# Kernel optimization log

Hardware: AMD Instinct MI355X
Metric: run time of the kernel (lower is better)

Reference implementation:

```python
import jax, jax.numpy as jnp
import numpy as np

B, BINS, EMBED, HID, IND = 1, 500, 1024, 512, 128
POOL, MC_CROP, HIC_CROP = 5, 50, 10


def setup_inputs() -> dict:
    key = jax.random.key(0)
    ks = jax.random.split(key, 10)
    def w(k, shape, fan_in):
        return (jax.random.normal(k, shape, jnp.float32) / np.sqrt(fan_in)).astype(jnp.float32)
    return dict(
        x=jax.random.normal(ks[0], (B, BINS, EMBED), jnp.float32),
        # project MLP
        p_w1=w(ks[1], (EMBED, HID), EMBED), p_b1=jnp.zeros((HID,), jnp.float32),
        p_w2=w(ks[2], (HID, HID), HID), p_b2=jnp.zeros((HID,), jnp.float32),
        # pairattn_cop stub: per-pair linears (micro at full res, hic after 5x5 avg-pool)
        micro_w=w(ks[3], (HID, IND), HID), micro_b=jnp.zeros((IND,), jnp.float32),
        hic_w=w(ks[4], (HID, IND), HID), hic_b=jnp.zeros((IND,), jnp.float32),
        # prediction heads
        head_mc_w=w(ks[5], (IND, 2), IND), head_mc_b=jnp.zeros((2,), jnp.float32),
        head_ih_w1=w(ks[6], (IND, IND // 2), IND), head_ih_b1=jnp.zeros((IND // 2,), jnp.float32),
        head_ih_w2=w(ks[7], (IND // 2, 2), IND // 2), head_ih_b2=jnp.zeros((2,), jnp.float32),
        head_hic_w=w(ks[8], (IND, 3), IND), head_hic_b=jnp.zeros((3,), jnp.float32),
    )


def reference(x, p_w1, p_b1, p_w2, p_b2, micro_w, micro_b, hic_w, hic_b,
              head_mc_w, head_mc_b, head_ih_w1, head_ih_b1, head_ih_w2, head_ih_b2,
              head_hic_w, head_hic_b):
    # project: Linear -> ReLU -> Linear
    h = jax.nn.relu(x @ p_w1 + p_b1) @ p_w2 + p_b2            # [B, bins, HID]
    # output_head: fused pairwise outer-sum mean + scaled elementwise dot
    xi = h[:, :, None, :]                                      # [B, bins, 1, HID]
    xj = h[:, None, :, :]                                      # [B, 1, bins, HID]
    pair = (xi + xj) * 0.5 + xi * xj * (1.0 / np.sqrt(HID))    # [B, bins, bins, HID]
    # pairattn_cop stub
    micro = pair @ micro_w + micro_b                           # [B, bins, bins, IND]
    nb = BINS // POOL
    hic_in = pair.reshape(B, nb, POOL, nb, POOL, HID).mean(axis=(2, 4))  # [B, nb, nb, HID]
    hic = hic_in @ hic_w + hic_b                               # [B, nb, nb, IND]
    # prediction heads with crops
    mc = micro[:, MC_CROP:-MC_CROP, MC_CROP:-MC_CROP, :]       # [B, 400, 400, IND]
    out_mc = mc @ head_mc_w + head_mc_b
    out_ih = jax.nn.relu(mc @ head_ih_w1 + head_ih_b1) @ head_ih_w2 + head_ih_b2
    hc = hic[:, HIC_CROP:-HIC_CROP, HIC_CROP:-HIC_CROP, :]     # [B, 80, 80, IND]
    out_hic = hc @ head_hic_w + head_hic_b
    return (out_mc, out_ih, micro, out_hic)
```

## Files before the change

kernel.cpp:

```cpp
#include <hip/hip_runtime.h>

#define BINS 500
#define HID  512
#define INDD 128
#define PAIR_S 0.044194173824159216f

#define OFF_MC    0
#define OFF_IH    320000
#define OFF_MICRO 640000
#define OFF_HIC   32640000

#define WS_U     0
#define WS_MWT   64000
#define WS_HBF   96768
#define WS_H     256000
#define WS_HBAR  512000
#define WS_HWT   563200
#define WS_W1CT  595968

typedef __bf16 bf16;
typedef bf16 bf16x4 __attribute__((ext_vector_type(4)));
typedef bf16 bf16x8 __attribute__((ext_vector_type(8)));
typedef float f32x4 __attribute__((ext_vector_type(4)));

__device__ __forceinline__ bf16x8 join8(bf16x4 lo, bf16x4 hi) {
  return __builtin_shufflevector(lo, hi, 0, 1, 2, 3, 4, 5, 6, 7);
}
__device__ __forceinline__ bf16x4 cvt4(float a, float b, float c, float d) {
  bf16x4 r; r[0] = (bf16)a; r[1] = (bf16)b; r[2] = (bf16)c; r[3] = (bf16)d; return r;
}

__global__ __launch_bounds__(256, 2)
void gemm_ks(const float* __restrict__ A, const float* __restrict__ B,
             const float* __restrict__ abias, float* __restrict__ C,
             int M, int N, int K_per, int a_relu, float scale) {
  __shared__ float a_lds[64][36];
  __shared__ float bt_lds[64][36];
  const int t = threadIdx.x;
  const int w = t >> 6, l = t & 63;
  const int lr = l & 15, g = l >> 4;
  const int r0 = blockIdx.x * 64, n0 = blockIdx.y * 64;
  const int kbase = blockIdx.z * K_per;
  f32x4 acc[4] = {};
  for (int kq = 0; kq < K_per; kq += 32) {
    const int k0 = kbase + kq;
    {
      int row = t >> 2, kc = (t & 3) * 8;
      int gr = r0 + row; gr = gr < M ? gr : M - 1;
      const float* src = A + (size_t)gr * K_per * gridDim.z + k0 + kc;
      float4 v0 = *(const float4*)src;
      float4 v1 = *(const float4*)(src + 4);
      if (abias) {
        const float* bp = abias + k0 + kc;
        v0.x += bp[0]; v0.y += bp[1]; v0.z += bp[2]; v0.w += bp[3];
        v1.x += bp[4]; v1.y += bp[5]; v1.z += bp[6]; v1.w += bp[7];
        if (a_relu) {
          v0.x = fmaxf(v0.x, 0.f); v0.y = fmaxf(v0.y, 0.f);
          v0.z = fmaxf(v0.z, 0.f); v0.w = fmaxf(v0.w, 0.f);
          v1.x = fmaxf(v1.x, 0.f); v1.y = fmaxf(v1.y, 0.f);
          v1.z = fmaxf(v1.z, 0.f); v1.w = fmaxf(v1.w, 0.f);
        }
      }
      *(float4*)&a_lds[row][kc]     = v0;
      *(float4*)&a_lds[row][kc + 4] = v1;
    }
    {
      int n = t & 63, ks = (t >> 6) * 8;
      const float* src = B + (size_t)(k0 + ks) * N + n0 + n;
      #pragma unroll
      for (int s = 0; s < 8; s++) bt_lds[n][ks + s] = src[(size_t)s * N];
    }
    __syncthreads();
    bf16x8 ahi, alo;
    {
      int row = w * 16 + lr;
      float4 u0 = *(const float4*)&a_lds[row][g * 8];
      float4 u1 = *(const float4*)&a_lds[row][g * 8 + 4];
      float v[8] = {u0.x, u0.y, u0.z, u0.w, u1.x, u1.y, u1.z, u1.w};
      #pragma unroll
      for (int e = 0; e < 8; e++) {
        bf16 h = (bf16)v[e];
        ahi[e] = h; alo[e] = (bf16)(v[e] - (float)h);
      }
    }
    #pragma unroll
    for (int fn = 0; fn < 4; fn++) {
      int col = fn * 16 + lr;
      float4 u0 = *(const float4*)&bt_lds[col][g * 8];
      float4 u1 = *(const float4*)&bt_lds[col][g * 8 + 4];
      float v[8] = {u0.x, u0.y, u0.z, u0.w, u1.x, u1.y, u1.z, u1.w};
      bf16x8 bhi, blo;
      #pragma unroll
      for (int e = 0; e < 8; e++) {
        bf16 h = (bf16)v[e];
        bhi[e] = h; blo[e] = (bf16)(v[e] - (float)h);
      }
      acc[fn] = __builtin_amdgcn_mfma_f32_16x16x32_bf16(ahi, bhi, acc[fn], 0, 0, 0);
      acc[fn] = __builtin_amdgcn_mfma_f32_16x16x32_bf16(ahi, blo, acc[fn], 0, 0, 0);
      acc[fn] = __builtin_amdgcn_mfma_f32_16x16x32_bf16(alo, bhi, acc[fn], 0, 0, 0);
    }
    __syncthreads();
  }
  #pragma unroll
  for (int fn = 0; fn < 4; fn++) {
    int col = n0 + fn * 16 + lr;
    #pragma unroll
    for (int r = 0; r < 4; r++) {
      int row = r0 + w * 16 + g * 4 + r;
      if (row < M) atomicAdd(&C[(size_t)row * N + col], acc[fn][r] * scale);
    }
  }
}

__global__ void post_h(const float* __restrict__ h, const float* __restrict__ b2,
                       const float* __restrict__ micro_w,
                       const float* __restrict__ hic_w, const float* __restrict__ w_ih1,
                       const float* __restrict__ w_mc, float* __restrict__ ws) {
  int g = blockIdx.x * 256 + threadIdx.x;
  if (g < 256000) {
    bf16* hbf = (bf16*)(ws + WS_HBF);
    int k = g & (HID - 1);
    hbf[g] = (bf16)(h[g] + b2[k]);
  } else if (g < 256000 + 65536) {
    int gg = g - 256000;
    int n = gg >> 9, k = gg & 511;
    bf16* mwt = (bf16*)(ws + WS_MWT);
    mwt[gg] = (bf16)(PAIR_S * micro_w[k * INDD + n]);
  } else if (g < 256000 + 65536 + 51200) {
    int gg = g - (256000 + 65536);
    int a = gg >> 9, k = gg & (HID - 1);
    const float* p = h + (size_t)(a * 5) * HID + k;
    ws[WS_HBAR + gg] = 0.2f * (p[0] + p[HID] + p[2 * HID] + p[3 * HID] + p[4 * HID]) + b2[k];
  } else if (g < 256000 + 65536 + 51200 + 65536) {
    int gg = g - (256000 + 65536 + 51200);
    int n = gg >> 9, k = gg & 511;
    bf16* hwt = (bf16*)(ws + WS_HWT);
    hwt[gg] = (bf16)hic_w[k * INDD + n];
  } else if (g < 256000 + 65536 + 51200 + 65536 + 10240) {
    int gg = g - (256000 + 65536 + 51200 + 65536);
    int n = gg >> 7, k = gg & 127;
    float v = 0.f;
    if (n < 64) v = w_ih1[k * 64 + n];
    else if (n < 66) v = w_mc[k * 2 + (n - 64)];
    bf16* w1c = (bf16*)(ws + WS_W1CT);
    w1c[gg] = (bf16)v;
  }
}

__global__ __launch_bounds__(256, 3)
void fused_micro(const float* __restrict__ wsf, const float* __restrict__ micro_b,
                 float* __restrict__ out) {
  __shared__ bf16 Ht[2][128 * 32];
  __shared__ bf16 Bt[2][128 * 32];
  const int t = threadIdx.x;
  const int wv = t >> 6, l = t & 63;
  const int wj = wv >> 1, wn = wv & 1;
  const int lr = l & 15, g = l >> 4;
  const int i  = blockIdx.x;
  const int j0 = blockIdx.y * 128;
  const bf16* Hbf = (const bf16*)(wsf + WS_HBF);
  const bf16* mwt = (const bf16*)(wsf + WS_MWT);
  const float* U  = wsf + WS_U;
  const int bn = t >> 1, bh = t & 1;
  const int arow   = l >> 2;
  const int achunk = (l & 3) ^ ((l >> 3) & 3);
  const bf16* hbi = Hbf + (size_t)i * HID;
  f32x4 acc[4][4] = {};

  #pragma unroll
  for (int q = 0; q < 2; q++) {
    int row = wv * 32 + q * 16 + arow;
    int jj = j0 + row; jj = jj < BINS ? jj : BINS - 1;
    const bf16* src = Hbf + (size_t)jj * HID + achunk * 8;
    __builtin_amdgcn_global_load_lds(
        (const __attribute__((address_space(1))) void*)src,
        (__attribute__((address_space(3))) void*)(&Ht[0][(wv * 32 + q * 16) * 32]),
        16, 0, 0);
  }
  {
    bf16x8 w0 = *(const bf16x8*)(mwt + (size_t)bn * HID + bh * 16);
    bf16x8 w1 = *(const bf16x8*)(mwt + (size_t)bn * HID + bh * 16 + 8);
    bf16x8 h0 = *(const bf16x8*)(hbi + bh * 16);
    bf16x8 h1 = *(const bf16x8*)(hbi + bh * 16 + 8);
    bf16x8 o0, o1;
    #pragma unroll
    for (int e = 0; e < 8; e++) o0[e] = (bf16)((float)h0[e] * (float)w0[e]);
    #pragma unroll
    for (int e = 0; e < 8; e++) o1[e] = (bf16)((float)h1[e] * (float)w1[e]);
    const int sw = (bn >> 1) & 3;
    *(bf16x8*)(&Bt[0][0] + bn * 32 + ((bh * 2)     ^ sw) * 8) = o0;
    *(bf16x8*)(&Bt[0][0] + bn * 32 + ((bh * 2 + 1) ^ sw) * 8) = o1;
  }
  asm volatile("s_waitcnt vmcnt(0) lgkmcnt(0)" ::: "memory");
  __builtin_amdgcn_s_barrier();

  int cur = 0;
  for (int kt = 0; kt < 16; kt++) {
    const bf16* htc = &Ht[cur][0];
    const bf16* btc = &Bt[cur][0];
    bf16x8 w0, w1, h0, h1;
    if (kt < 15) {
      const int kn = (kt + 1) * 32;
      w0 = *(const bf16x8*)(mwt + (size_t)bn * HID + kn + bh * 16);
      w1 = *(const bf16x8*)(mwt + (size_t)bn * HID + kn + bh * 16 + 8);
      h0 = *(const bf16x8*)(hbi + kn + bh * 16);
      h1 = *(const bf16x8*)(hbi + kn + bh * 16 + 8);
      #pragma unroll
      for (int q = 0; q < 2; q++) {
        int row = wv * 32 + q * 16 + arow;
        int jj = j0 + row; jj = jj < BINS ? jj : BINS - 1;
        const bf16* src = Hbf + (size_t)jj * HID + kn + achunk * 8;
        __builtin_amdgcn_global_load_lds(
            (const __attribute__((address_space(1))) void*)src,
            (__attribute__((address_space(3))) void*)(&Ht[cur ^ 1][(wv * 32 + q * 16) * 32]),
            16, 0, 0);
      }
      asm volatile("s_waitcnt vmcnt(6)" ::: "memory");
    } else {
      asm volatile("s_waitcnt vmcnt(0)" ::: "memory");
    }
    bf16x8 af[4], bfr[4];
    const int s = g ^ ((lr >> 1) & 3);
    #pragma unroll
    for (int fm = 0; fm < 4; fm++)
      af[fm] = *(const bf16x8*)(htc + (wj * 64 + fm * 16 + lr) * 32 + s * 8);
    #pragma unroll
    for (int fn = 0; fn < 4; fn++)
      bfr[fn] = *(const bf16x8*)(btc + (wn * 64 + fn * 16 + lr) * 32 + s * 8);
    #pragma unroll
    for (int fm = 0; fm < 4; fm++)
      #pragma unroll
      for (int fn = 0; fn < 4; fn++)
        acc[fm][fn] = __builtin_amdgcn_mfma_f32_16x16x32_bf16(af[fm], bfr[fn], acc[fm][fn], 0, 0, 0);
    if (kt < 15) {
      bf16x8 o0, o1;
      #pragma unroll
      for (int e = 0; e < 8; e++) o0[e] = (bf16)((float)h0[e] * (float)w0[e]);
      #pragma unroll
      for (int e = 0; e < 8; e++) o1[e] = (bf16)((float)h1[e] * (float)w1[e]);
      bf16* btn = &Bt[cur ^ 1][0];
      const int sw = (bn >> 1) & 3;
      *(bf16x8*)(btn + bn * 32 + ((bh * 2)     ^ sw) * 8) = o0;
      *(bf16x8*)(btn + bn * 32 + ((bh * 2 + 1) ^ sw) * 8) = o1;
    }
    asm volatile("s_waitcnt lgkmcnt(0)" ::: "memory");
    __builtin_amdgcn_s_barrier();
    cur ^= 1;
  }

  float Ui[4];
  #pragma unroll
  for (int fn = 0; fn < 4; fn++) {
    int n = wn * 64 + fn * 16 + lr;
    Ui[fn] = U[(size_t)i * INDD + n] + micro_b[n];
  }
  #pragma unroll
  for (int fm = 0; fm < 4; fm++) {
    #pragma unroll
    for (int r = 0; r < 4; r++) {
      int j = j0 + wj * 64 + fm * 16 + g * 4 + r;
      if (j < BINS) {
        const float* Uj = U + (size_t)j * INDD;
        size_t base = (size_t)OFF_MICRO + ((size_t)i * BINS + j) * INDD;
        #pragma unroll
        for (int fn = 0; fn < 4; fn++) {
          int n = wn * 64 + fn * 16 + lr;
          out[base + n] = acc[fm][fn][r] + Ui[fn] + Uj[n];
        }
      }
    }
  }
}

__global__ __launch_bounds__(256, 2)
void heads_kernel(const float* __restrict__ micro, const float* __restrict__ wsf,
                  const float* __restrict__ b1, const float* __restrict__ w2,
                  const float* __restrict__ bmc, const float* __restrict__ b2,
                  float* __restrict__ out) {
  __shared__ bf16 a_lds[256][36];
  __shared__ bf16 bt_lds[80][132];
  const int t = threadIdx.x;
  const int wv = t >> 6, l = t & 63;
  const int lr = l & 15, g = l >> 4;
  const int mm0 = blockIdx.x * 256;
  const bf16* w1c = (const bf16*)(wsf + WS_W1CT);
  for (int c = t; c < 1280; c += 256) {
    int n = c >> 4, part = c & 15;
    bf16x8 v = *(const bf16x8*)(w1c + n * 128 + part * 8);
    *(bf16x4*)&bt_lds[n][part * 8]     = __builtin_shufflevector(v, v, 0, 1, 2, 3);
    *(bf16x4*)&bt_lds[n][part * 8 + 4] = __builtin_shufflevector(v, v, 4, 5, 6, 7);
  }
  f32x4 acc[4][5] = {};
  const int mm = mm0 + t;
  const int ii = 50 + mm / 400, jj = 50 + mm % 400;
  const float* arow = micro + (size_t)(ii * BINS + jj) * INDD;
  for (int kt = 0; kt < 4; kt++) {
    {
      const float* src = arow + kt * 32;
      #pragma unroll
      for (int c = 0; c < 4; c++) {
        float4 v0 = *(const float4*)(src + c * 8);
        float4 v1 = *(const float4*)(src + c * 8 + 4);
        *(bf16x4*)&a_lds[t][c * 8]     = cvt4(v0.x, v0.y, v0.z, v0.w);
        *(bf16x4*)&a_lds[t][c * 8 + 4] = cvt4(v1.x, v1.y, v1.z, v1.w);
      }
    }
    __syncthreads();
    bf16x8 af[4], bfr[5];
    #pragma unroll
    for (int fm = 0; fm < 4; fm++) {
      int row = wv * 64 + fm * 16 + lr;
      af[fm] = join8(*(const bf16x4*)&a_lds[row][g * 8],
                     *(const bf16x4*)&a_lds[row][g * 8 + 4]);
    }
    #pragma unroll
    for (int fn = 0; fn < 5; fn++) {
      int n = fn * 16 + lr;
      bfr[fn] = join8(*(const bf16x4*)&bt_lds[n][kt * 32 + g * 8],
                      *(const bf16x4*)&bt_lds[n][kt * 32 + g * 8 + 4]);
    }
    #pragma unroll
    for (int fm = 0; fm < 4; fm++)
      #pragma unroll
      for (int fn = 0; fn < 5; fn++)
        acc[fm][fn] = __builtin_amdgcn_mfma_f32_16x16x32_bf16(af[fm], bfr[fn], acc[fm][fn], 0, 0, 0);
    __syncthreads();
  }
  float w2a[4], w2b[4], b1v[4];
  #pragma unroll
  for (int fn = 0; fn < 4; fn++) {
    int q = fn * 16 + lr;
    w2a[fn] = w2[q * 2]; w2b[fn] = w2[q * 2 + 1]; b1v[fn] = b1[q];
  }
  float bm = (lr < 2) ? bmc[lr] : 0.f;
  float b2a = b2[0], b2bv = b2[1];
  #pragma unroll
  for (int fm = 0; fm < 4; fm++) {
    #pragma unroll
    for (int r = 0; r < 4; r++) {
      int m = wv * 64 + fm * 16 + g * 4 + r;
      float s0 = 0.f, s1 = 0.f;
      #pragma unroll
      for (int fn = 0; fn < 4; fn++) {
        float v = fmaxf(acc[fm][fn][r] + b1v[fn], 0.f);
        s0 += v * w2a[fn]; s1 += v * w2b[fn];
      }
      #pragma unroll
      for (int mk = 1; mk < 16; mk <<= 1) {
        s0 += __shfl_xor(s0, mk);
        s1 += __shfl_xor(s1, mk);
      }
      size_t mo = (size_t)(mm0 + m);
      if (lr == 0) {
        out[OFF_IH + mo * 2]     = s0 + b2a;
        out[OFF_IH + mo * 2 + 1] = s1 + b2bv;
      }
      if (lr < 2) out[OFF_MC + mo * 2 + lr] = acc[fm][4][r] + bm;
    }
  }
}

__device__ __forceinline__ bf16x4 pair4(float4 a, float4 b) {
  bf16x4 r;
  r[0] = (bf16)((a.x + b.x) * 0.5f + a.x * b.x * PAIR_S);
  r[1] = (bf16)((a.y + b.y) * 0.5f + a.y * b.y * PAIR_S);
  r[2] = (bf16)((a.z + b.z) * 0.5f + a.z * b.z * PAIR_S);
  r[3] = (bf16)((a.w + b.w) * 0.5f + a.w * b.w * PAIR_S);
  return r;
}

__global__ __launch_bounds__(256, 2)
void hic_kernel(const float* __restrict__ hbar, const float* __restrict__ wsf,
                const float* __restrict__ hicb, const float* __restrict__ whic,
                const float* __restrict__ bhic, float* __restrict__ out) {
  __shared__ float ha_lds[16][36];
  __shared__ float hb_lds[16][36];
  __shared__ bf16 pair_lds[256][36];
  __shared__ bf16 bt_lds[128][36];
  const int t = threadIdx.x;
  const int wv = t >> 6, l = t & 63;
  const int lr = l & 15, g = l >> 4;
  const int a0 = 10 + blockIdx.x * 16, b0 = 10 + blockIdx.y * 16;
  const bf16* hwt = (const bf16*)(wsf + WS_HWT);
  f32x4 acc[4][8] = {};
  for (int kt = 0; kt < 16; kt++) {
    const int k0 = kt * 32;
    if (t < 64) {
      int row = t >> 2, c = (t & 3) * 8;
      const float* src = hbar + (size_t)(a0 + row) * HID + k0 + c;
      *(float4*)&ha_lds[row][c]     = *(const float4*)src;
      *(float4*)&ha_lds[row][c + 4] = *(const float4*)(src + 4);
    } else if (t < 128) {
      int tt = t - 64;
      int row = tt >> 2, c = (tt & 3) * 8;
      const float* src = hbar + (size_t)(b0 + row) * HID + k0 + c;
      *(float4*)&hb_lds[row][c]     = *(const float4*)src;
      *(float4*)&hb_lds[row][c + 4] = *(const float4*)(src + 4);
    } else {
      int tt = t - 128;
      #pragma unroll
      for (int rep = 0; rep < 4; rep++) {
        int chunk = tt * 4 + rep;
        int n = chunk >> 2, part = chunk & 3;
        bf16x8 v = *(const bf16x8*)(hwt + (size_t)n * HID + k0 + part * 8);
        *(bf16x4*)&bt_lds[n][part * 8]     = __builtin_shufflevector(v, v, 0, 1, 2, 3);
        *(bf16x4*)&bt_lds[n][part * 8 + 4] = __builtin_shufflevector(v, v, 4, 5, 6, 7);
      }
    }
    __syncthreads();
    {
      int m = t;
      const float* pa = &ha_lds[m >> 4][0];
      const float* pb = &hb_lds[m & 15][0];
      #pragma unroll
      for (int c = 0; c < 4; c++) {
        float4 av0 = *(const float4*)(pa + c * 8);
        float4 av1 = *(const float4*)(pa + c * 8 + 4);
        float4 bv0 = *(const float4*)(pb + c * 8);
        float4 bv1 = *(const float4*)(pb + c * 8 + 4);
        *(bf16x4*)&pair_lds[m][c * 8]     = pair4(av0, bv0);
        *(bf16x4*)&pair_lds[m][c * 8 + 4] = pair4(av1, bv1);
      }
    }
    __syncthreads();
    bf16x8 af[4], bfr[8];
    #pragma unroll
    for (int fm = 0; fm < 4; fm++) {
      int row = wv * 64 + fm * 16 + lr;
      af[fm] = join8(*(const bf16x4*)&pair_lds[row][g * 8],
                     *(const bf16x4*)&pair_lds[row][g * 8 + 4]);
    }
    #pragma unroll
    for (int fn = 0; fn < 8; fn++) {
      int col = fn * 16 + lr;
      bfr[fn] = join8(*(const bf16x4*)&bt_lds[col][g * 8],
                      *(const bf16x4*)&bt_lds[col][g * 8 + 4]);
    }
    #pragma unroll
    for (int fm = 0; fm < 4; fm++)
      #pragma unroll
      for (int fn = 0; fn < 8; fn++)
        acc[fm][fn] = __builtin_amdgcn_mfma_f32_16x16x32_bf16(af[fm], bfr[fn], acc[fm][fn], 0, 0, 0);
    __syncthreads();
  }
  float wh0[8], wh1[8], wh2[8], hbv[8];
  #pragma unroll
  for (int fn = 0; fn < 8; fn++) {
    int n = fn * 16 + lr;
    wh0[fn] = whic[n * 3]; wh1[fn] = whic[n * 3 + 1]; wh2[fn] = whic[n * 3 + 2];
    hbv[fn] = hicb[n];
  }
  float bh0 = bhic[0], bh1 = bhic[1], bh2 = bhic[2];
  #pragma unroll
  for (int fm = 0; fm < 4; fm++) {
    #pragma unroll
    for (int r = 0; r < 4; r++) {
      int m = wv * 64 + fm * 16 + g * 4 + r;
      float s0 = 0.f, s1 = 0.f, s2 = 0.f;
      #pragma unroll
      for (int fn = 0; fn < 8; fn++) {
        float v = acc[fm][fn][r] + hbv[fn];
        s0 += v * wh0[fn]; s1 += v * wh1[fn]; s2 += v * wh2[fn];
      }
      #pragma unroll
      for (int mk = 1; mk < 16; mk <<= 1) {
        s0 += __shfl_xor(s0, mk);
        s1 += __shfl_xor(s1, mk);
        s2 += __shfl_xor(s2, mk);
      }
      if (lr == 0) {
        int aa = a0 + (m >> 4) - 10, bb = b0 + (m & 15) - 10;
        size_t o = (size_t)OFF_HIC + (size_t)(aa * 80 + bb) * 3;
        out[o] = s0 + bh0; out[o + 1] = s1 + bh1; out[o + 2] = s2 + bh2;
      }
    }
  }
}

extern "C" void kernel_launch(void* const* d_in, const int* in_sizes, int n_in,
                              void* d_out, int out_size, void* d_ws, size_t ws_size,
                              hipStream_t stream) {
  (void)in_sizes; (void)n_in; (void)out_size; (void)ws_size;
  const float* x    = (const float*)d_in[0];
  const float* pw1  = (const float*)d_in[1];
  const float* pb1  = (const float*)d_in[2];
  const float* pw2  = (const float*)d_in[3];
  const float* pb2  = (const float*)d_in[4];
  const float* mw   = (const float*)d_in[5];
  const float* mb   = (const float*)d_in[6];
  const float* hw   = (const float*)d_in[7];
  const float* hb   = (const float*)d_in[8];
  const float* wmc  = (const float*)d_in[9];
  const float* bmc  = (const float*)d_in[10];
  const float* wih1 = (const float*)d_in[11];
  const float* bih1 = (const float*)d_in[12];
  const float* wih2 = (const float*)d_in[13];
  const float* bih2 = (const float*)d_in[14];
  const float* whic = (const float*)d_in[15];
  const float* bhic = (const float*)d_in[16];
  float* out = (float*)d_out;
  float* ws  = (float*)d_ws;

  hipMemsetAsync(ws, 0, 256000 * sizeof(float), stream);
  hipMemsetAsync(ws + WS_H, 0, 256000 * sizeof(float), stream);
  gemm_ks<<<dim3(8, 8, 4), 256, 0, stream>>>(x, pw1, nullptr, ws, 500, 512, 256, 0, 1.f);
  gemm_ks<<<dim3(8, 8, 2), 256, 0, stream>>>(ws, pw2, pb1, ws + WS_H, 500, 512, 256, 1, 1.f);
  hipMemsetAsync(ws + WS_U, 0, 64000 * sizeof(float), stream);
  post_h<<<1752, 256, 0, stream>>>(ws + WS_H, pb2, mw, hw, wih1, wmc, ws);
  gemm_ks<<<dim3(8, 2, 4), 256, 0, stream>>>(ws + WS_H, mw, pb2, ws + WS_U, 500, 128, 128, 0, 0.5f);
  fused_micro<<<dim3(500, 4), 256, 0, stream>>>(ws, mb, out);
  heads_kernel<<<625, 256, 0, stream>>>(out + OFF_MICRO, ws, bih1, wih2, bmc, bih2, out);
  hic_kernel<<<dim3(5, 5), 256, 0, stream>>>(ws + WS_HBAR, ws, hb, whic, bhic, out);
}
```

Measured before the change: 171.0 us.

## Precompute per-row scaled micro weights and stream them via global_load_lds

```diff
diff --git a/kernel.cpp b/kernel.cpp
--- a/kernel.cpp
+++ b/kernel.cpp
@@ -17,6 +17,8 @@
 #define WS_HBAR  512000
 #define WS_HWT   563200
 #define WS_W1CT  595968
+#define WS_BP    601088
+#define WS_TOTAL_FLOATS (601088 + 8388608)
 
 typedef __bf16 bf16;
 typedef bf16 bf16x4 __attribute__((ext_vector_type(4)));
@@ -28,6 +30,13 @@
 }
 __device__ __forceinline__ bf16x4 cvt4(float a, float b, float c, float d) {
   bf16x4 r; r[0] = (bf16)a; r[1] = (bf16)b; r[2] = (bf16)c; r[3] = (bf16)d; return r;
+}
+
+__global__ void zero_init(float* __restrict__ ws) {
+  int idx = (blockIdx.x * 256 + threadIdx.x) * 4;
+  float4 z = {0.f, 0.f, 0.f, 0.f};
+  *(float4*)(ws + idx) = z;
+  *(float4*)(ws + WS_H + idx) = z;
 }
 
 __global__ __launch_bounds__(256, 2)
@@ -144,12 +153,131 @@
     else if (n < 66) v = w_mc[k * 2 + (n - 64)];
     bf16* w1c = (bf16*)(ws + WS_W1CT);
     w1c[gg] = (bf16)v;
+  } else if (g < 256000 + 65536 + 51200 + 65536 + 10240 + 64000) {
+    int gg = g - (256000 + 65536 + 51200 + 65536 + 10240);
+    ws[WS_U + gg] = 0.f;
+  }
+}
+
+__global__ void bp_gen(const float* __restrict__ wsf, float* __restrict__ wso) {
+  const bf16* hbf = (const bf16*)(wsf + WS_HBF);
+  const bf16* mwt = (const bf16*)(wsf + WS_MWT);
+  bf16* bp = (bf16*)(wso + WS_BP);
+  int gid = blockIdx.x * 256 + threadIdx.x;
+  int i  = gid >> 13;
+  int rem = gid & 8191;
+  int n  = rem >> 6;
+  int kc = (rem & 63) * 8;
+  bf16x8 hv = *(const bf16x8*)(hbf + (size_t)i * HID + kc);
+  bf16x8 wv = *(const bf16x8*)(mwt + (size_t)n * HID + kc);
+  bf16x8 o;
+  #pragma unroll
+  for (int e = 0; e < 8; e++) o[e] = (bf16)((float)hv[e] * (float)wv[e]);
+  *(bf16x8*)(bp + (size_t)i * 65536 + (size_t)n * HID + kc) = o;
+}
+
+__global__ __launch_bounds__(256, 4)
+void fused_micro_pre(const float* __restrict__ wsf, const float* __restrict__ micro_b,
+                     float* __restrict__ out) {
+  __shared__ bf16 Ht[2][128 * 32];
+  __shared__ bf16 Bt[2][128 * 32];
+  const int t = threadIdx.x;
+  const int wv = t >> 6, l = t & 63;
+  const int wj = wv >> 1, wn = wv & 1;
+  const int lr = l & 15, g = l >> 4;
+  const int i  = blockIdx.x;
+  const int j0 = blockIdx.y * 128;
+  const bf16* Hbf = (const bf16*)(wsf + WS_HBF);
+  const bf16* bpi = (const bf16*)(wsf + WS_BP) + (size_t)i * 65536;
+  const float* U  = wsf + WS_U;
+  const int arow   = l >> 2;
+  const int achunk = (l & 3) ^ ((l >> 3) & 3);
+  f32x4 acc[4][4] = {};
+
+  #pragma unroll
+  for (int q = 0; q < 2; q++) {
+    int row = wv * 32 + q * 16 + arow;
+    int jj = j0 + row; jj = jj < BINS ? jj : BINS - 1;
+    __builtin_amdgcn_global_load_lds(
+        (const __attribute__((address_space(1))) void*)(Hbf + (size_t)jj * HID + achunk * 8),
+        (__attribute__((address_space(3))) void*)(&Ht[0][(wv * 32 + q * 16) * 32]),
+        16, 0, 0);
+    __builtin_amdgcn_global_load_lds(
+        (const __attribute__((address_space(1))) void*)(bpi + (size_t)row * HID + achunk * 8),
+        (__attribute__((address_space(3))) void*)(&Bt[0][(wv * 32 + q * 16) * 32]),
+        16, 0, 0);
+  }
+  asm volatile("s_waitcnt vmcnt(0)" ::: "memory");
+  __builtin_amdgcn_s_barrier();
+
+  int cur = 0;
+  for (int kt = 0; kt < 16; kt++) {
+    const bf16* htc = &Ht[cur][0];
+    const bf16* btc = &Bt[cur][0];
+    if (kt < 15) {
+      const int kn = (kt + 1) * 32;
+      #pragma unroll
+      for (int q = 0; q < 2; q++) {
+        int row = wv * 32 + q * 16 + arow;
+        int jj = j0 + row; jj = jj < BINS ? jj : BINS - 1;
+        __builtin_amdgcn_global_load_lds(
+            (const __attribute__((address_space(1))) void*)(Hbf + (size_t)jj * HID + kn + achunk * 8),
+            (__attribute__((address_space(3))) void*)(&Ht[cur ^ 1][(wv * 32 + q * 16) * 32]),
+            16, 0, 0);
+        __builtin_amdgcn_global_load_lds(
+            (const __attribute__((address_space(1))) void*)(bpi + (size_t)row * HID + kn + achunk * 8),
+            (__attribute__((address_space(3))) void*)(&Bt[cur ^ 1][(wv * 32 + q * 16) * 32]),
+            16, 0, 0);
+      }
+      asm volatile("s_waitcnt vmcnt(4)" ::: "memory");
+    } else {
+      asm volatile("s_waitcnt vmcnt(0)" ::: "memory");
+    }
+    bf16x8 af[4], bfr[4];
+    const int s = g ^ ((lr >> 1) & 3);
+    #pragma unroll
+    for (int fm = 0; fm < 4; fm++)
+      af[fm] = *(const bf16x8*)(htc + (wj * 64 + fm * 16 + lr) * 32 + s * 8);
+    #pragma unroll
+    for (int fn = 0; fn < 4; fn++)
+      bfr[fn] = *(const bf16x8*)(btc + (wn * 64 + fn * 16 + lr) * 32 + s * 8);
+    #pragma unroll
+    for (int fm = 0; fm < 4; fm++)
+      #pragma unroll
+      for (int fn = 0; fn < 4; fn++)
+        acc[fm][fn] = __builtin_amdgcn_mfma_f32_16x16x32_bf16(af[fm], bfr[fn], acc[fm][fn], 0, 0, 0);
+    asm volatile("s_waitcnt lgkmcnt(0)" ::: "memory");
+    __builtin_amdgcn_s_barrier();
+    cur ^= 1;
+  }
+
+  float Ui[4];
+  #pragma unroll
+  for (int fn = 0; fn < 4; fn++) {
+    int n = wn * 64 + fn * 16 + lr;
+    Ui[fn] = U[(size_t)i * INDD + n] + micro_b[n];
+  }
+  #pragma unroll
+  for (int fm = 0; fm < 4; fm++) {
+    #pragma unroll
+    for (int r = 0; r < 4; r++) {
+      int j = j0 + wj * 64 + fm * 16 + g * 4 + r;
+      if (j < BINS) {
+        const float* Uj = U + (size_t)j * INDD;
+        size_t base = (size_t)OFF_MICRO + ((size_t)i * BINS + j) * INDD;
+        #pragma unroll
+        for (int fn = 0; fn < 4; fn++) {
+          int n = wn * 64 + fn * 16 + lr;
+          out[base + n] = acc[fm][fn][r] + Ui[fn] + Uj[n];
+        }
+      }
+    }
   }
 }
 
 __global__ __launch_bounds__(256, 3)
-void fused_micro(const float* __restrict__ wsf, const float* __restrict__ micro_b,
-                 float* __restrict__ out) {
+void fused_micro_fb(const float* __restrict__ wsf, const float* __restrict__ micro_b,
+                    float* __restrict__ out) {
   __shared__ bf16 Ht[2][128 * 32];
   __shared__ bf16 Bt[2][128 * 32];
   const int t = threadIdx.x;
@@ -171,9 +299,8 @@
   for (int q = 0; q < 2; q++) {
     int row = wv * 32 + q * 16 + arow;
     int jj = j0 + row; jj = jj < BINS ? jj : BINS - 1;
-    const bf16* src = Hbf + (size_t)jj * HID + achunk * 8;
     __builtin_amdgcn_global_load_lds(
-        (const __attribute__((address_space(1))) void*)src,
+        (const __attribute__((address_space(1))) void*)(Hbf + (size_t)jj * HID + achunk * 8),
         (__attribute__((address_space(3))) void*)(&Ht[0][(wv * 32 + q * 16) * 32]),
         16, 0, 0);
   }
@@ -209,9 +336,8 @@
       for (int q = 0; q < 2; q++) {
         int row = wv * 32 + q * 16 + arow;
         int jj = j0 + row; jj = jj < BINS ? jj : BINS - 1;
-        const bf16* src = Hbf + (size_t)jj * HID + kn + achunk * 8;
         __builtin_amdgcn_global_load_lds(
-            (const __attribute__((address_space(1))) void*)src,
+            (const __attribute__((address_space(1))) void*)(Hbf + (size_t)jj * HID + kn + achunk * 8),
             (__attribute__((address_space(3))) void*)(&Ht[cur ^ 1][(wv * 32 + q * 16) * 32]),
             16, 0, 0);
       }
@@ -480,7 +606,7 @@
 extern "C" void kernel_launch(void* const* d_in, const int* in_sizes, int n_in,
                               void* d_out, int out_size, void* d_ws, size_t ws_size,
                               hipStream_t stream) {
-  (void)in_sizes; (void)n_in; (void)out_size; (void)ws_size;
+  (void)in_sizes; (void)n_in; (void)out_size;
   const float* x    = (const float*)d_in[0];
   const float* pw1  = (const float*)d_in[1];
   const float* pb1  = (const float*)d_in[2];
@@ -500,15 +626,16 @@
   const float* bhic = (const float*)d_in[16];
   float* out = (float*)d_out;
   float* ws  = (float*)d_ws;
-
-  hipMemsetAsync(ws, 0, 256000 * sizeof(float), stream);
-  hipMemsetAsync(ws + WS_H, 0, 256000 * sizeof(float), stream);
+  const bool use_bp = ws_size >= (size_t)WS_TOTAL_FLOATS * sizeof(float);
+
+  zero_init<<<250, 256, 0, stream>>>(ws);
   gemm_ks<<<dim3(8, 8, 4), 256, 0, stream>>>(x, pw1, nullptr, ws, 500, 512, 256, 0, 1.f);
   gemm_ks<<<dim3(8, 8, 2), 256, 0, stream>>>(ws, pw2, pb1, ws + WS_H, 500, 512, 256, 1, 1.f);
-  hipMemsetAsync(ws + WS_U, 0, 64000 * sizeof(float), stream);
-  post_h<<<1752, 256, 0, stream>>>(ws + WS_H, pb2, mw, hw, wih1, wmc, ws);
+  post_h<<<2252, 256, 0, stream>>>(ws + WS_H, pb2, mw, hw, wih1, wmc, ws);
+  if (use_bp) bp_gen<<<16384, 256, 0, stream>>>(ws, ws);
   gemm_ks<<<dim3(8, 2, 4), 256, 0, stream>>>(ws + WS_H, mw, pb2, ws + WS_U, 500, 128, 128, 0, 0.5f);
-  fused_micro<<<dim3(500, 4), 256, 0, stream>>>(ws, mb, out);
+  if (use_bp) fused_micro_pre<<<dim3(500, 4), 256, 0, stream>>>(ws, mb, out);
+  else        fused_micro_fb<<<dim3(500, 4), 256, 0, stream>>>(ws, mb, out);
   heads_kernel<<<625, 256, 0, stream>>>(out + OFF_MICRO, ws, bih1, wih2, bmc, bih2, out);
   hic_kernel<<<dim3(5, 5), 256, 0, stream>>>(ws + WS_HBAR, ws, hb, whic, bhic, out);
 }
```

Result: slower. 183.1 us (+7.0%).

## Fuse prediction heads into micro GEMM epilogue and replace memsets with kernels

Applied to the files above, without the earlier changes.

```diff
diff --git a/kernel.cpp b/kernel.cpp
--- a/kernel.cpp
+++ b/kernel.cpp
@@ -28,6 +28,13 @@
 }
 __device__ __forceinline__ bf16x4 cvt4(float a, float b, float c, float d) {
   bf16x4 r; r[0] = (bf16)a; r[1] = (bf16)b; r[2] = (bf16)c; r[3] = (bf16)d; return r;
+}
+
+__global__ void zero_init(float* __restrict__ ws) {
+  int idx = (blockIdx.x * 256 + threadIdx.x) * 4;
+  float4 z = {0.f, 0.f, 0.f, 0.f};
+  *(float4*)(ws + idx) = z;
+  *(float4*)(ws + WS_H + idx) = z;
 }
 
 __global__ __launch_bounds__(256, 2)
@@ -144,14 +151,18 @@
     else if (n < 66) v = w_mc[k * 2 + (n - 64)];
     bf16* w1c = (bf16*)(ws + WS_W1CT);
     w1c[gg] = (bf16)v;
+  } else if (g < 256000 + 65536 + 51200 + 65536 + 10240 + 64000) {
+    int gg = g - (256000 + 65536 + 51200 + 65536 + 10240);
+    ws[WS_U + gg] = 0.f;
   }
 }
 
 __global__ __launch_bounds__(256, 3)
-void fused_micro(const float* __restrict__ wsf, const float* __restrict__ micro_b,
-                 float* __restrict__ out) {
-  __shared__ bf16 Ht[2][128 * 32];
-  __shared__ bf16 Bt[2][128 * 32];
+void fused_micro_heads(const float* __restrict__ wsf, const float* __restrict__ micro_b,
+                       const float* __restrict__ b1, const float* __restrict__ w2,
+                       const float* __restrict__ bmc, const float* __restrict__ b2,
+                       float* __restrict__ out) {
+  __shared__ bf16 smem[16384];
   const int t = threadIdx.x;
   const int wv = t >> 6, l = t & 63;
   const int wj = wv >> 1, wn = wv & 1;
@@ -171,10 +182,9 @@
   for (int q = 0; q < 2; q++) {
     int row = wv * 32 + q * 16 + arow;
     int jj = j0 + row; jj = jj < BINS ? jj : BINS - 1;
-    const bf16* src = Hbf + (size_t)jj * HID + achunk * 8;
     __builtin_amdgcn_global_load_lds(
-        (const __attribute__((address_space(1))) void*)src,
-        (__attribute__((address_space(3))) void*)(&Ht[0][(wv * 32 + q * 16) * 32]),
+        (const __attribute__((address_space(1))) void*)(Hbf + (size_t)jj * HID + achunk * 8),
+        (__attribute__((address_space(3))) void*)(smem + (wv * 32 + q * 16) * 32),
         16, 0, 0);
   }
   {
@@ -188,16 +198,16 @@
     #pragma unroll
     for (int e = 0; e < 8; e++) o1[e] = (bf16)((float)h1[e] * (float)w1[e]);
     const int sw = (bn >> 1) & 3;
-    *(bf16x8*)(&Bt[0][0] + bn * 32 + ((bh * 2)     ^ sw) * 8) = o0;
-    *(bf16x8*)(&Bt[0][0] + bn * 32 + ((bh * 2 + 1) ^ sw) * 8) = o1;
+    *(bf16x8*)(smem + 8192 + bn * 32 + ((bh * 2)     ^ sw) * 8) = o0;
+    *(bf16x8*)(smem + 8192 + bn * 32 + ((bh * 2 + 1) ^ sw) * 8) = o1;
   }
   asm volatile("s_waitcnt vmcnt(0) lgkmcnt(0)" ::: "memory");
   __builtin_amdgcn_s_barrier();
 
   int cur = 0;
   for (int kt = 0; kt < 16; kt++) {
-    const bf16* htc = &Ht[cur][0];
-    const bf16* btc = &Bt[cur][0];
+    const bf16* htc = smem + cur * 4096;
+    const bf16* btc = smem + 8192 + cur * 4096;
     bf16x8 w0, w1, h0, h1;
     if (kt < 15) {
       const int kn = (kt + 1) * 32;
@@ -209,10 +219,9 @@
       for (int q = 0; q < 2; q++) {
         int row = wv * 32 + q * 16 + arow;
         int jj = j0 + row; jj = jj < BINS ? jj : BINS - 1;
-        const bf16* src = Hbf + (size_t)jj * HID + kn + achunk * 8;
         __builtin_amdgcn_global_load_lds(
-            (const __attribute__((address_space(1))) void*)src,
-            (__attribute__((address_space(3))) void*)(&Ht[cur ^ 1][(wv * 32 + q * 16) * 32]),
+            (const __attribute__((address_space(1))) void*)(Hbf + (size_t)jj * HID + kn + achunk * 8),
+            (__attribute__((address_space(3))) void*)(smem + (cur ^ 1) * 4096 + (wv * 32 + q * 16) * 32),
             16, 0, 0);
       }
       asm volatile("s_waitcnt vmcnt(6)" ::: "memory");
@@ -238,7 +247,7 @@
       for (int e = 0; e < 8; e++) o0[e] = (bf16)((float)h0[e] * (float)w0[e]);
       #pragma unroll
       for (int e = 0; e < 8; e++) o1[e] = (bf16)((float)h1[e] * (float)w1[e]);
-      bf16* btn = &Bt[cur ^ 1][0];
+      bf16* btn = smem + 8192 + (cur ^ 1) * 4096;
       const int sw = (bn >> 1) & 3;
       *(bf16x8*)(btn + bn * 32 + ((bh * 2)     ^ sw) * 8) = o0;
       *(bf16x8*)(btn + bn * 32 + ((bh * 2 + 1) ^ sw) * 8) = o1;
@@ -258,104 +267,82 @@
   for (int fm = 0; fm < 4; fm++) {
     #pragma unroll
     for (int r = 0; r < 4; r++) {
-      int j = j0 + wj * 64 + fm * 16 + g * 4 + r;
-      if (j < BINS) {
-        const float* Uj = U + (size_t)j * INDD;
-        size_t base = (size_t)OFF_MICRO + ((size_t)i * BINS + j) * INDD;
+      int j_local = wj * 64 + fm * 16 + g * 4 + r;
+      int j = j0 + j_local;
+      int jc = j < BINS ? j : BINS - 1;
+      const float* Uj = U + (size_t)jc * INDD;
+      size_t base = (size_t)OFF_MICRO + ((size_t)i * BINS + jc) * INDD;
+      #pragma unroll
+      for (int fn = 0; fn < 4; fn++) {
+        int n = wn * 64 + fn * 16 + lr;
+        float vv = acc[fm][fn][r] + Ui[fn] + Uj[n];
+        if (j < BINS) out[base + n] = vv;
+        smem[j_local * 128 + ((((n >> 3) ^ (j_local & 7))) << 3) + (n & 7)] = (bf16)vv;
+      }
+    }
+  }
+  asm volatile("s_waitcnt lgkmcnt(0)" ::: "memory");
+  __builtin_amdgcn_s_barrier();
+
+  if (i >= 50 && i < 450) {
+    const bf16* w1c = (const bf16*)(wsf + WS_W1CT);
+    f32x4 acc2[2][5] = {};
+    const int jg = wv * 32;
+    #pragma unroll
+    for (int kt2 = 0; kt2 < 4; kt2++) {
+      const int k0 = kt2 * 32;
+      bf16x8 bfr[5];
+      #pragma unroll
+      for (int fn = 0; fn < 5; fn++) {
+        int q = fn * 16 + lr;
+        bfr[fn] = *(const bf16x8*)(w1c + q * 128 + k0 + g * 8);
+      }
+      bf16x8 af2[2];
+      #pragma unroll
+      for (int s16 = 0; s16 < 2; s16++) {
+        int row = jg + s16 * 16 + lr;
+        int chunk = (k0 >> 3) + g;
+        af2[s16] = *(const bf16x8*)(smem + row * 128 + ((chunk ^ (row & 7)) << 3));
+      }
+      #pragma unroll
+      for (int s16 = 0; s16 < 2; s16++)
+        #pragma unroll
+        for (int fn = 0; fn < 5; fn++)
+          acc2[s16][fn] = __builtin_amdgcn_mfma_f32_16x16x32_bf16(af2[s16], bfr[fn], acc2[s16][fn], 0, 0, 0);
+    }
+    float w2a[4], w2b[4], b1v[4];
+    #pragma unroll
+    for (int fn = 0; fn < 4; fn++) {
+      int q = fn * 16 + lr;
+      w2a[fn] = w2[q * 2]; w2b[fn] = w2[q * 2 + 1]; b1v[fn] = b1[q];
+    }
+    float bm = (lr < 2) ? bmc[lr] : 0.f;
+    float b2a = b2[0], b2bv = b2[1];
+    #pragma unroll
+    for (int s16 = 0; s16 < 2; s16++) {
+      #pragma unroll
+      for (int r = 0; r < 4; r++) {
+        int j = j0 + jg + s16 * 16 + g * 4 + r;
+        float s0 = 0.f, s1 = 0.f;
         #pragma unroll
         for (int fn = 0; fn < 4; fn++) {
-          int n = wn * 64 + fn * 16 + lr;
-          out[base + n] = acc[fm][fn][r] + Ui[fn] + Uj[n];
+          float v = fmaxf(acc2[s16][fn][r] + b1v[fn], 0.f);
+          s0 += v * w2a[fn]; s1 += v * w2b[fn];
         }
-      }
-    }
-  }
-}
-
-__global__ __launch_bounds__(256, 2)
-void heads_kernel(const float* __restrict__ micro, const float* __restrict__ wsf,
-                  const float* __restrict__ b1, const float* __restrict__ w2,
-                  const float* __restrict__ bmc, const float* __restrict__ b2,
-                  float* __restrict__ out) {
-  __shared__ bf16 a_lds[256][36];
-  __shared__ bf16 bt_lds[80][132];
-  const int t = threadIdx.x;
-  const int wv = t >> 6, l = t & 63;
-  const int lr = l & 15, g = l >> 4;
-  const int mm0 = blockIdx.x * 256;
-  const bf16* w1c = (const bf16*)(wsf + WS_W1CT);
-  for (int c = t; c < 1280; c += 256) {
-    int n = c >> 4, part = c & 15;
-    bf16x8 v = *(const bf16x8*)(w1c + n * 128 + part * 8);
-    *(bf16x4*)&bt_lds[n][part * 8]     = __builtin_shufflevector(v, v, 0, 1, 2, 3);
-    *(bf16x4*)&bt_lds[n][part * 8 + 4] = __builtin_shufflevector(v, v, 4, 5, 6, 7);
-  }
-  f32x4 acc[4][5] = {};
-  const int mm = mm0 + t;
-  const int ii = 50 + mm / 400, jj = 50 + mm % 400;
-  const float* arow = micro + (size_t)(ii * BINS + jj) * INDD;
-  for (int kt = 0; kt < 4; kt++) {
-    {
-      const float* src = arow + kt * 32;
-      #pragma unroll
-      for (int c = 0; c < 4; c++) {
-        float4 v0 = *(const float4*)(src + c * 8);
-        float4 v1 = *(const float4*)(src + c * 8 + 4);
-        *(bf16x4*)&a_lds[t][c * 8]     = cvt4(v0.x, v0.y, v0.z, v0.w);
-        *(bf16x4*)&a_lds[t][c * 8 + 4] = cvt4(v1.x, v1.y, v1.z, v1.w);
-      }
-    }
-    __syncthreads();
-    bf16x8 af[4], bfr[5];
-    #pragma unroll
-    for (int fm = 0; fm < 4; fm++) {
-      int row = wv * 64 + fm * 16 + lr;
-      af[fm] = join8(*(const bf16x4*)&a_lds[row][g * 8],
-                     *(const bf16x4*)&a_lds[row][g * 8 + 4]);
-    }
-    #pragma unroll
-    for (int fn = 0; fn < 5; fn++) {
-      int n = fn * 16 + lr;
-      bfr[fn] = join8(*(const bf16x4*)&bt_lds[n][kt * 32 + g * 8],
-                      *(const bf16x4*)&bt_lds[n][kt * 32 + g * 8 + 4]);
-    }
-    #pragma unroll
-    for (int fm = 0; fm < 4; fm++)
-      #pragma unroll
-      for (int fn = 0; fn < 5; fn++)
-        acc[fm][fn] = __builtin_amdgcn_mfma_f32_16x16x32_bf16(af[fm], bfr[fn], acc[fm][fn], 0, 0, 0);
-    __syncthreads();
-  }
-  float w2a[4], w2b[4], b1v[4];
-  #pragma unroll
-  for (int fn = 0; fn < 4; fn++) {
-    int q = fn * 16 + lr;
-    w2a[fn] = w2[q * 2]; w2b[fn] = w2[q * 2 + 1]; b1v[fn] = b1[q];
-  }
-  float bm = (lr < 2) ? bmc[lr] : 0.f;
-  float b2a = b2[0], b2bv = b2[1];
-  #pragma unroll
-  for (int fm = 0; fm < 4; fm++) {
-    #pragma unroll
-    for (int r = 0; r < 4; r++) {
-      int m = wv * 64 + fm * 16 + g * 4 + r;
-      float s0 = 0.f, s1 = 0.f;
-      #pragma unroll
-      for (int fn = 0; fn < 4; fn++) {
-        float v = fmaxf(acc[fm][fn][r] + b1v[fn], 0.f);
-        s0 += v * w2a[fn]; s1 += v * w2b[fn];
-      }
-      #pragma unroll
-      for (int mk = 1; mk < 16; mk <<= 1) {
-        s0 += __shfl_xor(s0, mk);
-        s1 += __shfl_xor(s1, mk);
-      }
-      size_t mo = (size_t)(mm0 + m);
-      if (lr == 0) {
-        out[OFF_IH + mo * 2]     = s0 + b2a;
-        out[OFF_IH + mo * 2 + 1] = s1 + b2bv;
-      }
-      if (lr < 2) out[OFF_MC + mo * 2 + lr] = acc[fm][4][r] + bm;
+        #pragma unroll
+        for (int mk = 1; mk < 16; mk <<= 1) {
+          s0 += __shfl_xor(s0, mk);
+          s1 += __shfl_xor(s1, mk);
+        }
+        if (j >= 50 && j < 450) {
+          size_t mo = (size_t)(i - 50) * 400 + (j - 50);
+          if (lr == 0) {
+            out[OFF_IH + mo * 2]     = s0 + b2a;
+            out[OFF_IH + mo * 2 + 1] = s1 + b2bv;
+          }
+          if (lr < 2) out[OFF_MC + mo * 2 + lr] = acc2[s16][4][r] + bm;
+        }
+      }
     }
   }
 }
@@ -501,14 +488,11 @@
   float* out = (float*)d_out;
   float* ws  = (float*)d_ws;
 
-  hipMemsetAsync(ws, 0, 256000 * sizeof(float), stream);
-  hipMemsetAsync(ws + WS_H, 0, 256000 * sizeof(float), stream);
+  zero_init<<<250, 256, 0, stream>>>(ws);
   gemm_ks<<<dim3(8, 8, 4), 256, 0, stream>>>(x, pw1, nullptr, ws, 500, 512, 256, 0, 1.f);
   gemm_ks<<<dim3(8, 8, 2), 256, 0, stream>>>(ws, pw2, pb1, ws + WS_H, 500, 512, 256, 1, 1.f);
-  hipMemsetAsync(ws + WS_U, 0, 64000 * sizeof(float), stream);
-  post_h<<<1752, 256, 0, stream>>>(ws + WS_H, pb2, mw, hw, wih1, wmc, ws);
+  post_h<<<2252, 256, 0, stream>>>(ws + WS_H, pb2, mw, hw, wih1, wmc, ws);
   gemm_ks<<<dim3(8, 2, 4), 256, 0, stream>>>(ws + WS_H, mw, pb2, ws + WS_U, 500, 128, 128, 0, 0.5f);
-  fused_micro<<<dim3(500, 4), 256, 0, stream>>>(ws, mb, out);
-  heads_kernel<<<625, 256, 0, stream>>>(out + OFF_MICRO, ws, bih1, wih2, bmc, bih2, out);
+  fused_micro_heads<<<dim3(500, 4), 256, 0, stream>>>(ws, mb, bih1, wih2, bmc, bih2, out);
   hic_kernel<<<dim3(5, 5), 256, 0, stream>>>(ws + WS_HBAR, ws, hb, whic, bhic, out);
 }
```

New measurement: 169.3 us. Within noise of the previous version (-1.0%).
